# Optimization experiments

Measured on AMD Instinct MI355X. Metric: run time of the kernel, lower is better.

The kernel has to match this reference:

```python
import jax, jax.numpy as jnp
import numpy as np

# DeformConv1d config (matches init_kwargs)
K = 3          # kernel_size
DIL = 1        # dilation
STRIDE = 1
PAD = DIL * (K - 1)  # 'same' total padding = 2 -> (1,1) reflect


def setup_inputs() -> dict:
    key = jax.random.key(0)
    k1, k2, k3, k4 = jax.random.split(key, 4)
    B, C, L = 16, 64, 8192
    O = 64
    x = jax.random.normal(k1, (B, C, L), dtype=jnp.float32)
    offsets = jax.random.normal(k2, (B, 1, L, K), dtype=jnp.float32)
    weight = jax.random.normal(k3, (O, C, K), dtype=jnp.float32) * (1.0 / np.sqrt(C * K))
    bias = jax.random.normal(k4, (O,), dtype=jnp.float32) * 0.01
    return {"x": x, "offsets": offsets, "weight": weight, "bias": bias}


def _deform_conv1d(x, offsets, weight, bias):
    # reflect 'same' padding: left = PAD//2, right = PAD - PAD//2
    left = PAD // 2
    x_pad = jnp.pad(x, ((0, 0), (0, 0), (left, PAD - left)), mode="reflect")
    B, C, Lp = x_pad.shape
    OL = offsets.shape[-2]
    dt = x.dtype

    dilated = (jnp.arange(K, dtype=dt) * DIL)          # [K] = [0, d, ..., d(K-1)]
    t0 = (jnp.arange(OL, dtype=dt) * STRIDE)[:, None]  # [OL, 1]

    # sampling positions T: [B, G, OL, K], constrained to kernel receptive field
    T = t0 + dilated + offsets
    T = jnp.maximum(T, t0)
    T = jnp.minimum(T, t0 + dilated[-1])

    # integer lower neighbors (no grad through floor); clamp so U+1 is valid
    U = jnp.clip(jnp.floor(T).astype(jnp.int32), 0, Lp - 2)  # [B, G, OL, K]

    # gather both neighbors along length axis (broadcast offset group -> C)
    idx = jnp.broadcast_to(U, (B, C, OL, K)).reshape(B, C, OL * K)
    x0 = jnp.take_along_axis(x_pad, idx, axis=2).reshape(B, C, OL, K)
    x1 = jnp.take_along_axis(x_pad, idx + 1, axis=2).reshape(B, C, OL, K)

    # linear interpolation weights G = max(0, 1 - |U - T|)
    Uf = U.astype(dt)
    w0 = jnp.maximum(0.0, 1.0 - jnp.abs(Uf - T))        # [B, G, OL, K]
    w1 = jnp.maximum(0.0, 1.0 - jnp.abs(Uf + 1.0 - T))
    sampled = w0 * x0 + w1 * x1                          # [B, C, OL, K]

    # conv1d(weight, stride=K) on flattened [B, C, OL*K] == per-position contraction
    out = jnp.einsum("bcok,fck->bfo", sampled, weight) + bias[None, :, None]
    return out


def reference(x, offsets, weight, bias):
    return _deform_conv1d(x, offsets, weight, bias)
```

## Files before the change

### kernel.cpp

```cpp
#include <hip/hip_runtime.h>
#include <stdint.h>

#define BB   16
#define CC   64
#define LL   8192
#define OO   64
#define KK   3
#define TT   64
#define XSW  72
#define SW   200

typedef __attribute__((ext_vector_type(8))) short short8;
typedef __attribute__((ext_vector_type(4))) float float4_t;

__device__ __forceinline__ ushort f2bf(float f) {
    uint32_t u = __float_as_uint(f);
    return (ushort)((u + 0x7FFFu + ((u >> 16) & 1u)) >> 16);
}
__device__ __forceinline__ float bf2f(ushort h) {
    return __uint_as_float(((uint32_t)h) << 16);
}

__global__ void wt_prep(const float* __restrict__ w, ushort* __restrict__ wt) {
    int idx = blockIdx.x * 256 + threadIdx.x;
    if (idx < OO * CC * KK) {
        int f = idx / (CC * KK);
        int rem = idx - f * (CC * KK);
        int c = rem / KK;
        int k = rem - c * KK;
        wt[f * (KK * CC) + k * CC + c] = f2bf(w[idx]);
    }
}

__global__ __launch_bounds__(256, 2) void deform_main(
    const float* __restrict__ x, const float* __restrict__ offs,
    const ushort* __restrict__ wt, const float* __restrict__ bias,
    float* __restrict__ out) {

    __shared__ ushort xs[67 * XSW];
    __shared__ ushort S[TT * SW];
    __shared__ ushort Wt[OO * SW];
    __shared__ int    Ul[TT * KK];
    __shared__ float  W0s[TT * KK], W1s[TT * KK];

    const int tid  = threadIdx.x;
    const int bb   = blockIdx.x >> 7;
    const int tile = blockIdx.x & 127;
    const int ts   = tile * TT;

    {
        const uint4* src = (const uint4*)wt;
        #pragma unroll
        for (int i = 0; i < 6; i++) {
            int idx = tid + i * 256;
            int e0  = idx * 8;
            int row = e0 / 192;
            int col = e0 - row * 192;
            *(uint4*)&Wt[row * SW + col] = src[idx];
        }
    }

    {
        const float* xb = x + (size_t)bb * (CC * LL);
        #pragma unroll
        for (int i = 0; i < 17; i++) {
            int idx = tid + i * 256;
            if (idx < 64 * 67) {
                int c = idx / 67;
                int p = idx - c * 67;
                int j = ts + p - 1;
                if (j < 0) j = -j;
                if (j >= LL) j = 2 * LL - 2 - j;
                xs[p * XSW + c] = f2bf(xb[c * LL + j]);
            }
        }
    }

    if (tid < TT * KK) {
        int n = tid / 3;
        int k = tid - n * 3;
        float off = offs[((size_t)bb * LL + ts + n) * 3 + k];
        float t0  = (float)(ts + n);
        float T   = t0 + (float)k + off;
        T = fmaxf(T, t0);
        T = fminf(T, t0 + 2.0f);
        int U = (int)floorf(T);
        if (U > LL) U = LL;
        float Uf = (float)U;
        float w0 = fmaxf(0.0f, 1.0f - fabsf(Uf - T));
        float w1 = fmaxf(0.0f, 1.0f - fabsf(Uf + 1.0f - T));
        Ul[tid]  = U - ts;
        W0s[tid] = w0;
        W1s[tid] = w1;
    }
    __syncthreads();

    #pragma unroll
    for (int i = 0; i < 6; i++) {
        int tau = tid + i * 256;
        int g   = tau & 7;
        int nk  = tau >> 3;
        int n   = nk / 3;
        int k   = nk - n * 3;
        int u   = Ul[nk];
        float w0 = W0s[nk], w1 = W1s[nk];
        int c0  = g * 8;
        union { uint4 v; ushort u16[8]; } r0, r1;
        r0.v = *(const uint4*)&xs[u * XSW + c0];
        r1.v = *(const uint4*)&xs[(u + 1) * XSW + c0];
        uint32_t pk[4];
        #pragma unroll
        for (int j = 0; j < 4; j++) {
            float v0 = w0 * bf2f(r0.u16[2 * j])     + w1 * bf2f(r1.u16[2 * j]);
            float v1 = w0 * bf2f(r0.u16[2 * j + 1]) + w1 * bf2f(r1.u16[2 * j + 1]);
            pk[j] = (uint32_t)f2bf(v0) | ((uint32_t)f2bf(v1) << 16);
        }
        uint4 ov;
        ov.x = pk[0]; ov.y = pk[1]; ov.z = pk[2]; ov.w = pk[3];
        *(uint4*)&S[n * SW + k * 64 + c0] = ov;
    }
    __syncthreads();

    const int lane = tid & 63;
    const int wv   = tid >> 6;
    const int lr   = lane & 15;
    const int q    = lane >> 4;
    float4_t acc0 = {0.f, 0.f, 0.f, 0.f};
    float4_t acc1 = acc0, acc2 = acc0, acc3 = acc0;

    #pragma unroll
    for (int kk = 0; kk < 6; kk++) {
        int k0 = kk * 32 + q * 8;
        short8 a  = *(const short8*)&Wt[(wv * 16 + lr) * SW + k0];
        short8 b0 = *(const short8*)&S[(0 * 16 + lr) * SW + k0];
        short8 b1 = *(const short8*)&S[(1 * 16 + lr) * SW + k0];
        short8 b2 = *(const short8*)&S[(2 * 16 + lr) * SW + k0];
        short8 b3 = *(const short8*)&S[(3 * 16 + lr) * SW + k0];
        acc0 = __builtin_amdgcn_mfma_f32_16x16x32_bf16(a, b0, acc0, 0, 0, 0);
        acc1 = __builtin_amdgcn_mfma_f32_16x16x32_bf16(a, b1, acc1, 0, 0, 0);
        acc2 = __builtin_amdgcn_mfma_f32_16x16x32_bf16(a, b2, acc2, 0, 0, 0);
        acc3 = __builtin_amdgcn_mfma_f32_16x16x32_bf16(a, b3, acc3, 0, 0, 0);
    }

    const int f0 = wv * 16 + q * 4;
    float4_t bv = *(const float4_t*)&bias[f0];
    float* ob = out + ((size_t)bb * OO + f0) * LL + ts;
    #pragma unroll
    for (int r = 0; r < 4; r++) {
        float* orow = ob + (size_t)r * LL;
        orow[ 0 + lr] = acc0[r] + bv[r];
        orow[16 + lr] = acc1[r] + bv[r];
        orow[32 + lr] = acc2[r] + bv[r];
        orow[48 + lr] = acc3[r] + bv[r];
    }
}

extern "C" void kernel_launch(void* const* d_in, const int* in_sizes, int n_in,
                              void* d_out, int out_size, void* d_ws, size_t ws_size,
                              hipStream_t stream) {
    const float* x    = (const float*)d_in[0];
    const float* offs = (const float*)d_in[1];
    const float* w    = (const float*)d_in[2];
    const float* bias = (const float*)d_in[3];
    float* out = (float*)d_out;
    ushort* wt = (ushort*)d_ws;

    hipLaunchKernelGGL(wt_prep, dim3((OO * CC * KK + 255) / 256), dim3(256), 0, stream, w, wt);
    hipLaunchKernelGGL(deform_main, dim3(BB * (LL / TT)), dim3(256), 0, stream,
                       x, offs, wt, bias, out);
}
```

Measured before the change: 106.5 us.

## Fuse interpolation into MFMA operand build and read weights from global

Removes the shared-memory staging of the sampled matrix S and the weight tile Wt. Each wave now interpolates its own B operand in registers right before the MFMA, and it reads A weight fragments directly from global (L1/L2 cached) memory. The wave-to-tile mapping changes so that each wave owns 16 output positions across all 64 filters. This cuts LDS use and one barrier, and the launch bounds are raised to 4 blocks per CU for higher occupancy. The cost is redundant global weight loads per block and possible register pressure.

```diff
diff --git a/kernel.cpp b/kernel.cpp
--- a/kernel.cpp
+++ b/kernel.cpp
@@ -8,7 +8,6 @@
 #define KK   3
 #define TT   64
 #define XSW  72
-#define SW   200
 
 typedef __attribute__((ext_vector_type(8))) short short8;
 typedef __attribute__((ext_vector_type(4))) float float4_t;
@@ -32,14 +31,12 @@
     }
 }
 
-__global__ __launch_bounds__(256, 2) void deform_main(
+__global__ __launch_bounds__(256, 4) void deform_main(
     const float* __restrict__ x, const float* __restrict__ offs,
     const ushort* __restrict__ wt, const float* __restrict__ bias,
     float* __restrict__ out) {
 
     __shared__ ushort xs[67 * XSW];
-    __shared__ ushort S[TT * SW];
-    __shared__ ushort Wt[OO * SW];
     __shared__ int    Ul[TT * KK];
     __shared__ float  W0s[TT * KK], W1s[TT * KK];
 
@@ -47,18 +44,6 @@
     const int bb   = blockIdx.x >> 7;
     const int tile = blockIdx.x & 127;
     const int ts   = tile * TT;
-
-    {
-        const uint4* src = (const uint4*)wt;
-        #pragma unroll
-        for (int i = 0; i < 6; i++) {
-            int idx = tid + i * 256;
-            int e0  = idx * 8;
-            int row = e0 / 192;
-            int col = e0 - row * 192;
-            *(uint4*)&Wt[row * SW + col] = src[idx];
-        }
-    }
 
     {
         const float* xb = x + (size_t)bb * (CC * LL);
@@ -87,37 +72,9 @@
         int U = (int)floorf(T);
         if (U > LL) U = LL;
         float Uf = (float)U;
-        float w0 = fmaxf(0.0f, 1.0f - fabsf(Uf - T));
-        float w1 = fmaxf(0.0f, 1.0f - fabsf(Uf + 1.0f - T));
         Ul[tid]  = U - ts;
-        W0s[tid] = w0;
-        W1s[tid] = w1;
-    }
-    __syncthreads();
-
-    #pragma unroll
-    for (int i = 0; i < 6; i++) {
-        int tau = tid + i * 256;
-        int g   = tau & 7;
-        int nk  = tau >> 3;
-        int n   = nk / 3;
-        int k   = nk - n * 3;
-        int u   = Ul[nk];
-        float w0 = W0s[nk], w1 = W1s[nk];
-        int c0  = g * 8;
-        union { uint4 v; ushort u16[8]; } r0, r1;
-        r0.v = *(const uint4*)&xs[u * XSW + c0];
-        r1.v = *(const uint4*)&xs[(u + 1) * XSW + c0];
-        uint32_t pk[4];
-        #pragma unroll
-        for (int j = 0; j < 4; j++) {
-            float v0 = w0 * bf2f(r0.u16[2 * j])     + w1 * bf2f(r1.u16[2 * j]);
-            float v1 = w0 * bf2f(r0.u16[2 * j + 1]) + w1 * bf2f(r1.u16[2 * j + 1]);
-            pk[j] = (uint32_t)f2bf(v0) | ((uint32_t)f2bf(v1) << 16);
-        }
-        uint4 ov;
-        ov.x = pk[0]; ov.y = pk[1]; ov.z = pk[2]; ov.w = pk[3];
-        *(uint4*)&S[n * SW + k * 64 + c0] = ov;
+        W0s[tid] = fmaxf(0.0f, 1.0f - fabsf(Uf - T));
+        W1s[tid] = fmaxf(0.0f, 1.0f - fabsf(Uf + 1.0f - T));
     }
     __syncthreads();
 
@@ -125,33 +82,50 @@
     const int wv   = tid >> 6;
     const int lr   = lane & 15;
     const int q    = lane >> 4;
+    const int n    = wv * 16 + lr;
+
     float4_t acc0 = {0.f, 0.f, 0.f, 0.f};
     float4_t acc1 = acc0, acc2 = acc0, acc3 = acc0;
 
     #pragma unroll
     for (int kk = 0; kk < 6; kk++) {
-        int k0 = kk * 32 + q * 8;
-        short8 a  = *(const short8*)&Wt[(wv * 16 + lr) * SW + k0];
-        short8 b0 = *(const short8*)&S[(0 * 16 + lr) * SW + k0];
-        short8 b1 = *(const short8*)&S[(1 * 16 + lr) * SW + k0];
-        short8 b2 = *(const short8*)&S[(2 * 16 + lr) * SW + k0];
-        short8 b3 = *(const short8*)&S[(3 * 16 + lr) * SW + k0];
-        acc0 = __builtin_amdgcn_mfma_f32_16x16x32_bf16(a, b0, acc0, 0, 0, 0);
-        acc1 = __builtin_amdgcn_mfma_f32_16x16x32_bf16(a, b1, acc1, 0, 0, 0);
-        acc2 = __builtin_amdgcn_mfma_f32_16x16x32_bf16(a, b2, acc2, 0, 0, 0);
-        acc3 = __builtin_amdgcn_mfma_f32_16x16x32_bf16(a, b3, acc3, 0, 0, 0);
+        const int k  = kk >> 1;
+        const int k0 = kk * 32 + q * 8;
+        const int c0 = k0 & 63;
+        const int nk = n * KK + k;
+        const int u  = Ul[nk];
+        const float w0 = W0s[nk], w1 = W1s[nk];
+        union { uint4 v; ushort u16[8]; } r0, r1;
+        r0.v = *(const uint4*)&xs[u * XSW + c0];
+        r1.v = *(const uint4*)&xs[(u + 1) * XSW + c0];
+        union { short8 s; uint32_t u32[4]; } bf;
+        #pragma unroll
+        for (int j = 0; j < 4; j++) {
+            float v0 = w0 * bf2f(r0.u16[2 * j])     + w1 * bf2f(r1.u16[2 * j]);
+            float v1 = w0 * bf2f(r0.u16[2 * j + 1]) + w1 * bf2f(r1.u16[2 * j + 1]);
+            bf.u32[j] = (uint32_t)f2bf(v0) | ((uint32_t)f2bf(v1) << 16);
+        }
+        short8 a0 = *(const short8*)&wt[(0 * 16 + lr) * (KK * CC) + k0];
+        short8 a1 = *(const short8*)&wt[(1 * 16 + lr) * (KK * CC) + k0];
+        short8 a2 = *(const short8*)&wt[(2 * 16 + lr) * (KK * CC) + k0];
+        short8 a3 = *(const short8*)&wt[(3 * 16 + lr) * (KK * CC) + k0];
+        acc0 = __builtin_amdgcn_mfma_f32_16x16x32_bf16(a0, bf.s, acc0, 0, 0, 0);
+        acc1 = __builtin_amdgcn_mfma_f32_16x16x32_bf16(a1, bf.s, acc1, 0, 0, 0);
+        acc2 = __builtin_amdgcn_mfma_f32_16x16x32_bf16(a2, bf.s, acc2, 0, 0, 0);
+        acc3 = __builtin_amdgcn_mfma_f32_16x16x32_bf16(a3, bf.s, acc3, 0, 0, 0);
     }
 
-    const int f0 = wv * 16 + q * 4;
-    float4_t bv = *(const float4_t*)&bias[f0];
-    float* ob = out + ((size_t)bb * OO + f0) * LL + ts;
+    const int col = ts + wv * 16 + lr;
+    float4_t accs[4] = {acc0, acc1, acc2, acc3};
     #pragma unroll
-    for (int r = 0; r < 4; r++) {
-        float* orow = ob + (size_t)r * LL;
-        orow[ 0 + lr] = acc0[r] + bv[r];
-        orow[16 + lr] = acc1[r] + bv[r];
-        orow[32 + lr] = acc2[r] + bv[r];
-        orow[48 + lr] = acc3[r] + bv[r];
+    for (int mt = 0; mt < 4; mt++) {
+        const int f0 = mt * 16 + q * 4;
+        float4_t bv = *(const float4_t*)&bias[f0];
+        float* ob = out + ((size_t)bb * OO + f0) * LL + col;
+        #pragma unroll
+        for (int r = 0; r < 4; r++) {
+            ob[(size_t)r * LL] = accs[mt][r] + bv[r];
+        }
     }
 }
 
```

Result: slower. 114.5 us (+7.5%).
